# Optimization experiments

Measured on AMD Instinct MI355X. Metric: run time of the kernel, lower is better.

The kernel has to match this reference:

```python
import jax, jax.numpy as jnp
import numpy as np
import math

INPUT_SIZE = 4096
NUM_NEURONS = 4096
ATTN_SIZE = 64
BATCH = 8192


def setup_inputs() -> dict:
    key = jax.random.key(0)
    ks = jax.random.split(key, 10)
    lim_in = 1.0 / math.sqrt(INPUT_SIZE)
    lim_a = 1.0 / math.sqrt(ATTN_SIZE)
    x = jax.random.normal(ks[0], (BATCH, INPUT_SIZE), dtype=jnp.float32)
    # attention linears (torch default uniform(-1/sqrt(fan_in), ...))
    Wq = jax.random.uniform(ks[1], (ATTN_SIZE, INPUT_SIZE), jnp.float32, -lim_in, lim_in)
    bq = jnp.zeros((ATTN_SIZE,), jnp.float32)
    Wk = jax.random.uniform(ks[2], (ATTN_SIZE, INPUT_SIZE), jnp.float32, -lim_in, lim_in)
    bk = jnp.zeros((ATTN_SIZE,), jnp.float32)
    Wv = jax.random.uniform(ks[3], (ATTN_SIZE, INPUT_SIZE), jnp.float32, -lim_in, lim_in)
    bv = jnp.zeros((ATTN_SIZE,), jnp.float32)
    Wo = jax.random.uniform(ks[4], (INPUT_SIZE, ATTN_SIZE), jnp.float32, -lim_a, lim_a)
    bo = jnp.zeros((INPUT_SIZE,), jnp.float32)
    # stacked single-weight neurons: weight ~ N(0,1)*0.01, bias 0
    Wn = jax.random.normal(ks[5], (NUM_NEURONS, INPUT_SIZE), jnp.float32) * 0.01
    bn = jnp.zeros((NUM_NEURONS,), jnp.float32)
    return {"x": x, "Wq": Wq, "bq": bq, "Wk": Wk, "bk": bk,
            "Wv": Wv, "bv": bv, "Wo": Wo, "bo": bo, "Wn": Wn, "bn": bn}


def reference(x, Wq, bq, Wk, bk, Wv, bv, Wo, bo, Wn, bn):
    scale = math.sqrt(ATTN_SIZE)
    # x is treated as a length-1 "sequence" of the full feature vector: [B, 1, S]
    q = x @ Wq.T + bq            # [B, A]
    k = x @ Wk.T + bk            # [B, A]
    v = x @ Wv.T + bv            # [B, A]
    # attention over a single token: softmax of a single score == 1, kept for fidelity
    scores = jnp.sum(q * k, axis=-1, keepdims=True) / scale      # [B, 1]
    attn_w = jax.nn.softmax(scores[:, :, None], axis=-1)          # [B, 1, 1] -> all ones
    attended = attn_w[:, 0, :] * v                                # [B, A] == v
    attn_out = attended @ Wo.T + bo                               # [B, S]
    h = attn_out + x                                              # residual
    # stacked single-weight neurons == one GEMM
    out = h @ Wn.T + bn                                           # [B, N]
    return jax.nn.relu(out)
```

## Files before the change

### kernel.cpp

```cpp
#include <hip/hip_runtime.h>
#include <stdint.h>


typedef unsigned short u16;
typedef float f32x4 __attribute__((ext_vector_type(4)));
typedef __bf16 bf16x8 __attribute__((ext_vector_type(8)));
typedef u16 u16x8 __attribute__((ext_vector_type(8)));

__device__ __forceinline__ float b2f(u16 u) {
  union { unsigned int i; float f; } x; x.i = ((unsigned int)u) << 16; return x.f;
}
__device__ __forceinline__ u16 f2b(float f) {
  union { float f; unsigned int i; } x; x.f = f;
  unsigned int r = x.i + 0x7FFFu + ((x.i >> 16) & 1u);
  return (u16)(r >> 16);
}

__device__ __forceinline__ void gl_lds16(const u16* g, u16* l) {
#if __has_builtin(__builtin_amdgcn_global_load_lds)
  __builtin_amdgcn_global_load_lds((__attribute__((address_space(1))) void*)g,
                                   (__attribute__((address_space(3))) void*)l, 16, 0, 0);
#else
  int lane = threadIdx.x & 63;
  *(u16x8*)(l + lane * 8) = *(const u16x8*)g;
#endif
}

__device__ __forceinline__ f32x4 mfma16(bf16x8 a, bf16x8 b, f32x4 c) {
  return __builtin_amdgcn_mfma_f32_16x16x32_bf16(a, b, c, 0, 0, 0);
}

#define XCH 4194304L
#define WNCH 2097152L
__global__ __launch_bounds__(256) void k_cvt(
    const float* __restrict__ x, const float* __restrict__ Wn, const float* __restrict__ Wv,
    u16* __restrict__ xb, u16* __restrict__ Wnb, u16* __restrict__ Wvb) {
  long i = (long)blockIdx.x * 256 + threadIdx.x;
  const float* src; u16* dst; long off;
  if (i < XCH) { src = x; dst = xb; off = i * 8; }
  else if (i < XCH + WNCH) { src = Wn; dst = Wnb; off = (i - XCH) * 8; }
  else { src = Wv; dst = Wvb; off = (i - XCH - WNCH) * 8; }
  f32x4 a = *(const f32x4*)&src[off];
  f32x4 b = *(const f32x4*)&src[off + 4];
  u16x8 o;
#pragma unroll
  for (int e = 0; e < 4; ++e) { o[e] = f2b(a[e]); o[4 + e] = f2b(b[e]); }
  *(u16x8*)&dst[off] = o;
}

__global__ __launch_bounds__(256) void kT(const float* __restrict__ Wo, u16* __restrict__ WoT) {
  __shared__ __align__(16) u16 t[64 * 72];
  const int b = blockIdx.x;
  const int tid = threadIdx.x;
  {
    int k = tid >> 2, a0 = (tid & 3) * 16;
    const float* src = &Wo[(size_t)(b * 64 + k) * 64 + a0];
#pragma unroll
    for (int q = 0; q < 4; ++q) {
      f32x4 v = *(const f32x4*)&src[q * 4];
#pragma unroll
      for (int e = 0; e < 4; ++e) t[k * 72 + a0 + q * 4 + e] = f2b(v[e]);
    }
  }
  __syncthreads();
  {
    int a = tid >> 2, k0 = (tid & 3) * 16;
    u16x8 o0, o1;
#pragma unroll
    for (int j = 0; j < 8; ++j) o0[j] = t[(k0 + j) * 72 + a];
#pragma unroll
    for (int j = 0; j < 8; ++j) o1[j] = t[(k0 + 8 + j) * 72 + a];
    *(u16x8*)&WoT[(size_t)a * 4096 + b * 64 + k0] = o0;
    *(u16x8*)&WoT[(size_t)a * 4096 + b * 64 + k0 + 8] = o1;
  }
}

#define PBK 128
__device__ void gemm_n64(const u16* __restrict__ A, const u16* __restrict__ B,
                         u16* __restrict__ C, const float* __restrict__ bias,
                         long m0, u16* lA, u16* lB) {
  const int tid = threadIdx.x;
  const int w = tid >> 6, l = tid & 63;
  f32x4 acc[4];
#pragma unroll
  for (int nt = 0; nt < 4; ++nt) acc[nt] = (f32x4)(0.f);

  for (int k0 = 0; k0 < 4096; k0 += PBK) {
    __syncthreads();
#pragma unroll
    for (int i = 0; i < 4; ++i) {
      int row = w * 16 + i * 4 + (l >> 4);
      int p = (l & 15) ^ (i * 4 + (l >> 4));
      gl_lds16(A + (m0 + row) * (long)4096 + k0 + p * 8, lA + (w * 16 + i * 4) * PBK);
      gl_lds16(B + (long)row * 4096 + k0 + p * 8, lB + (w * 16 + i * 4) * PBK);
    }
    __syncthreads();
#pragma unroll
    for (int kk = 0; kk < 4; ++kk) {
      int slotA = ((kk * 4 + (l >> 4)) ^ (l & 15)) * 8;
      bf16x8 af = *(const bf16x8*)&lA[(w * 16 + (l & 15)) * PBK + slotA];
#pragma unroll
      for (int nt = 0; nt < 4; ++nt) {
        bf16x8 bf = *(const bf16x8*)&lB[(nt * 16 + (l & 15)) * PBK + slotA];
        acc[nt] = mfma16(af, bf, acc[nt]);
      }
    }
  }
#pragma unroll
  for (int nt = 0; nt < 4; ++nt) {
    int col = nt * 16 + (l & 15);
    float bb = bias ? bias[col] : 0.f;
#pragma unroll
    for (int r = 0; r < 4; ++r) {
      long row = m0 + w * 16 + (l >> 4) * 4 + r;
      C[row * 64 + col] = f2b(acc[nt][r] + bb);
    }
  }
}

__global__ __launch_bounds__(256, 2) void k_prep(
    const u16* __restrict__ xb, const u16* __restrict__ Wvb, const float* __restrict__ bv,
    const u16* __restrict__ Wnb, const u16* __restrict__ WoT,
    const float* __restrict__ bo, const float* __restrict__ bn,
    u16* __restrict__ V, u16* __restrict__ Wm, float* __restrict__ biasTot) {
  __shared__ __align__(16) u16 lA[64 * PBK];
  __shared__ __align__(16) u16 lB[64 * PBK];
  const int bid = blockIdx.x;
  if (bid < 128) {
    gemm_n64(xb, Wvb, V, bv, (long)bid * 64, lA, lB);
  } else if (bid < 192) {
    gemm_n64(Wnb, WoT, Wm, nullptr, (long)(bid - 128) * 64, lA, lB);
  } else {
    const int w = threadIdx.x >> 6, l = threadIdx.x & 63;
    const int n = (bid - 192) * 4 + w;
    float s = 0.f;
#pragma unroll
    for (int j = 0; j < 8; ++j) {
      int off = (j * 64 + l) * 8;
      u16x8 a = *(const u16x8*)&Wnb[(size_t)n * 4096 + off];
      f32x4 c0 = *(const f32x4*)&bo[off];
      f32x4 c1 = *(const f32x4*)&bo[off + 4];
#pragma unroll
      for (int e = 0; e < 4; ++e) s += b2f(a[e]) * c0[e] + b2f(a[4 + e]) * c1[e];
    }
#pragma unroll
    for (int o = 32; o > 0; o >>= 1) s += __shfl_xor(s, o, 64);
    if (l == 0) biasTot[n] = s + bn[n];
  }
}

__global__ __launch_bounds__(256, 2) void k_main(
    const u16* __restrict__ X, const u16* __restrict__ Wn,
    const u16* __restrict__ V, const u16* __restrict__ Wm,
    const float* __restrict__ biasTot, float* __restrict__ Out) {
  __shared__ __align__(16) u16 smem[2 * 128 * 64];
  u16* lA = smem;
  u16* lB = smem + 128 * 64;
  const int tid = threadIdx.x;
  const int w = tid >> 6, l = tid & 63;
  const int wRow = (w & 1) * 64, wCol = (w >> 1) * 64;
  const long mBase = (long)(blockIdx.x >> 5) * 128;
  const int nBase = (int)(blockIdx.x & 31) * 128;

  f32x4 acc[4][4];
#pragma unroll
  for (int mt = 0; mt < 4; ++mt)
#pragma unroll
    for (int nt = 0; nt < 4; ++nt) acc[mt][nt] = (f32x4)(0.f);

  const int srow = l >> 3;
  const int sp = ((l & 7) ^ srow) * 8;

  for (int kb = 0; kb < 65; ++kb) {
    const u16 *pA, *pB; long lda;
    if (kb < 64) { pA = X + (long)kb * 64; pB = Wn + (long)kb * 64; lda = 4096; }
    else         { pA = V;                 pB = Wm;                 lda = 64;  }
    __syncthreads();
#pragma unroll
    for (int i = 0; i < 4; ++i) {
      int row = w * 32 + i * 8 + srow;
      gl_lds16(pA + (mBase + row) * lda + sp, lA + (w * 32 + i * 8) * 64);
      gl_lds16(pB + (long)(nBase + row) * lda + sp, lB + (w * 32 + i * 8) * 64);
    }
    __syncthreads();
#pragma unroll
    for (int kk = 0; kk < 2; ++kk) {
      int slot = ((kk * 4 + (l >> 4)) ^ (l & 7)) * 8;
      bf16x8 af[4], bfr[4];
#pragma unroll
      for (int mt = 0; mt < 4; ++mt)
        af[mt] = *(const bf16x8*)&lA[(wRow + mt * 16 + (l & 15)) * 64 + slot];
#pragma unroll
      for (int nt = 0; nt < 4; ++nt)
        bfr[nt] = *(const bf16x8*)&lB[(wCol + nt * 16 + (l & 15)) * 64 + slot];
#pragma unroll
      for (int mt = 0; mt < 4; ++mt)
#pragma unroll
        for (int nt = 0; nt < 4; ++nt) acc[mt][nt] = mfma16(af[mt], bfr[nt], acc[mt][nt]);
    }
  }

  __syncthreads();
  float* eb = ((float*)smem) + w * 1024;
#pragma unroll
  for (int mt = 0; mt < 4; ++mt) {
#pragma unroll
    for (int nt = 0; nt < 4; ++nt) {
      float bt = biasTot[nBase + wCol + nt * 16 + (l & 15)];
#pragma unroll
      for (int r = 0; r < 4; ++r) {
        float val = acc[mt][nt][r] + bt;
        eb[((l >> 4) * 4 + r) * 64 + nt * 16 + (l & 15)] = fmaxf(val, 0.f);
      }
    }
    int rr = l >> 2, c0 = (l & 3) * 16;
    long grow = mBase + wRow + mt * 16 + rr;
    int gcol = nBase + wCol + c0;
    f32x4 o0 = *(const f32x4*)&eb[rr * 64 + c0];
    f32x4 o1 = *(const f32x4*)&eb[rr * 64 + c0 + 4];
    f32x4 o2 = *(const f32x4*)&eb[rr * 64 + c0 + 8];
    f32x4 o3 = *(const f32x4*)&eb[rr * 64 + c0 + 12];
    *(f32x4*)&Out[grow * 4096 + gcol] = o0;
    *(f32x4*)&Out[grow * 4096 + gcol + 4] = o1;
    *(f32x4*)&Out[grow * 4096 + gcol + 8] = o2;
    *(f32x4*)&Out[grow * 4096 + gcol + 12] = o3;
  }
}

extern "C" void kernel_launch(void* const* d_in, const int* in_sizes, int n_in,
                              void* d_out, int out_size, void* d_ws, size_t ws_size,
                              hipStream_t stream) {
  const float* x  = (const float*)d_in[0];
  const float* Wv = (const float*)d_in[5];
  const float* bv = (const float*)d_in[6];
  const float* Wo = (const float*)d_in[7];
  const float* bo = (const float*)d_in[8];
  const float* Wn = (const float*)d_in[9];
  const float* bn = (const float*)d_in[10];
  float* out = (float*)d_out;

  char* ws = (char*)d_ws;
  u16* xb  = (u16*)ws;
  u16* Wnb = (u16*)(ws + (64L << 20));
  u16* Wvb = (u16*)(ws + (96L << 20));
  u16* WoT = (u16*)(ws + (96L << 20) + (512 << 10));
  u16* V   = (u16*)(ws + (97L << 20));
  u16* Wm  = (u16*)(ws + (98L << 20));
  float* biasTot = (float*)(ws + (98L << 20) + (512 << 10));

  k_cvt<<<dim3(24704), dim3(256), 0, stream>>>(x, Wn, Wv, xb, Wnb, Wvb);
  kT<<<dim3(64), dim3(256), 0, stream>>>(Wo, WoT);
  k_prep<<<dim3(1216), dim3(256), 0, stream>>>(xb, Wvb, bv, Wnb, WoT, bo, bn, V, Wm, biasTot);
  k_main<<<dim3(2048), dim3(256), 0, stream>>>(xb, Wnb, V, Wm, biasTot, out);
}
```

Baseline: 586.8 us.

## Restructure main GEMM to 256x256 tiles with a 4-stage LDS prefetch pipeline

The main bf16 GEMM moves from 128x128 tiles with 256 threads and a single-buffer load-sync-compute loop to 256x256 tiles with 512 threads. Each wave now holds a 128x64 accumulator. Global-to-LDS loads run two stages ahead through a 4-slot ring buffer, are split between the A and B halves, and are interleaved with MFMA phases raised via setprio. The goal is to hide global memory latency and reduce operand traffic per FLOP. The cost is 128KB of LDS per block, which limits occupancy to one block per CU, and a smaller grid of 512 blocks.

```diff
diff --git a/kernel.cpp b/kernel.cpp
--- a/kernel.cpp
+++ b/kernel.cpp
@@ -149,68 +149,126 @@
   }
 }
 
-__global__ __launch_bounds__(256, 2) void k_main(
+__global__ __launch_bounds__(512, 2) void k_main(
     const u16* __restrict__ X, const u16* __restrict__ Wn,
     const u16* __restrict__ V, const u16* __restrict__ Wm,
     const float* __restrict__ biasTot, float* __restrict__ Out) {
-  __shared__ __align__(16) u16 smem[2 * 128 * 64];
-  u16* lA = smem;
-  u16* lB = smem + 128 * 64;
+  __shared__ __align__(16) u16 smem[4 * 16384];
   const int tid = threadIdx.x;
   const int w = tid >> 6, l = tid & 63;
-  const int wRow = (w & 1) * 64, wCol = (w >> 1) * 64;
-  const long mBase = (long)(blockIdx.x >> 5) * 128;
-  const int nBase = (int)(blockIdx.x & 31) * 128;
-
-  f32x4 acc[4][4];
-#pragma unroll
-  for (int mt = 0; mt < 4; ++mt)
+  const int wm = w >> 2, wn = w & 3;
+  const long mBase = (long)(blockIdx.x >> 4) * 256;
+  const int  nBase = (int)(blockIdx.x & 15) * 256;
+
+  const int rs  = l >> 2;
+  const int gsl = ((l & 3) ^ ((l >> 3) & 3)) * 8;
+  const long rA = mBase + w * 16 + rs;
+  const long rB = nBase + w * 16 + rs;
+  const u16* xA0 = X  + rA * 4096 + gsl;
+  const u16* xA1 = xA0 + 128L * 4096;
+  const u16* nB0 = Wn + rB * 4096 + gsl;
+  const u16* nB1 = nB0 + 128L * 4096;
+  const u16* vA0 = V  + rA * 64 + gsl;
+  const u16* vA1 = vA0 + 128 * 64;
+  const u16* wB0 = Wm + rB * 64 + gsl;
+  const u16* wB1 = wB0 + 128 * 64;
+  const int dA0 = w * 512;
+  const int dA1 = 4096 + dA0;
+  const int dB0 = 8192 + dA0, dB1 = 8192 + dA1;
+
+  const int frow = l & 15;
+  const int sxor = ((l >> 4) ^ ((l >> 1) & 3)) * 8;
+  const int aoffA = (wm * 128 + frow) * 32 + sxor;
+  const int aoffB = 8192 + (wn * 64 + frow) * 32 + sxor;
+
+  f32x4 acc[8][4];
+#pragma unroll
+  for (int mt = 0; mt < 8; ++mt)
 #pragma unroll
     for (int nt = 0; nt < 4; ++nt) acc[mt][nt] = (f32x4)(0.f);
 
-  const int srow = l >> 3;
-  const int sp = ((l & 7) ^ srow) * 8;
-
-  for (int kb = 0; kb < 65; ++kb) {
-    const u16 *pA, *pB; long lda;
-    if (kb < 64) { pA = X + (long)kb * 64; pB = Wn + (long)kb * 64; lda = 4096; }
-    else         { pA = V;                 pB = Wm;                 lda = 64;  }
-    __syncthreads();
-#pragma unroll
-    for (int i = 0; i < 4; ++i) {
-      int row = w * 32 + i * 8 + srow;
-      gl_lds16(pA + (mBase + row) * lda + sp, lA + (w * 32 + i * 8) * 64);
-      gl_lds16(pB + (long)(nBase + row) * lda + sp, lB + (w * 32 + i * 8) * 64);
-    }
-    __syncthreads();
-#pragma unroll
-    for (int kk = 0; kk < 2; ++kk) {
-      int slot = ((kk * 4 + (l >> 4)) ^ (l & 7)) * 8;
-      bf16x8 af[4], bfr[4];
-#pragma unroll
-      for (int mt = 0; mt < 4; ++mt)
-        af[mt] = *(const bf16x8*)&lA[(wRow + mt * 16 + (l & 15)) * 64 + slot];
-#pragma unroll
-      for (int nt = 0; nt < 4; ++nt)
-        bfr[nt] = *(const bf16x8*)&lB[(wCol + nt * 16 + (l & 15)) * 64 + slot];
-#pragma unroll
-      for (int mt = 0; mt < 4; ++mt)
-#pragma unroll
-        for (int nt = 0; nt < 4; ++nt) acc[mt][nt] = mfma16(af[mt], bfr[nt], acc[mt][nt]);
-    }
+  gl_lds16(xA0,      smem + dA0);
+  gl_lds16(xA1,      smem + dA1);
+  gl_lds16(nB0,      smem + dB0);
+  gl_lds16(nB1,      smem + dB1);
+  gl_lds16(xA0 + 32, smem + 16384 + dA0);
+  gl_lds16(xA1 + 32, smem + 16384 + dA1);
+  gl_lds16(nB0 + 32, smem + 16384 + dB0);
+  gl_lds16(nB1 + 32, smem + 16384 + dB1);
+  asm volatile("s_waitcnt vmcnt(4)" ::: "memory");
+  __builtin_amdgcn_s_barrier();
+
+  bf16x8 af[4], bq[4];
+  for (int s = 0; s < 130; ++s) {
+    const int qb = (s & 3) * 16384;
+    const int t = s + 2;
+    const int qs = (t & 3) * 16384;
+    const long ko = (long)t * 32;
+#pragma unroll
+    for (int i = 0; i < 4; ++i) af[i] = *(const bf16x8*)&smem[qb + aoffA + i * 512];
+#pragma unroll
+    for (int i = 0; i < 4; ++i) bq[i] = *(const bf16x8*)&smem[qb + aoffB + i * 512];
+    if (t < 128) {
+      gl_lds16(xA0 + ko, smem + qs + dA0);
+      gl_lds16(xA1 + ko, smem + qs + dA1);
+    } else if (t < 130) {
+      const long kv = (long)(t - 128) * 32;
+      gl_lds16(vA0 + kv, smem + qs + dA0);
+      gl_lds16(vA1 + kv, smem + qs + dA1);
+    }
+    __builtin_amdgcn_s_barrier();
+    asm volatile("s_waitcnt lgkmcnt(0)" ::: "memory");
+    __builtin_amdgcn_sched_barrier(0);
+    __builtin_amdgcn_s_setprio(1);
+#pragma unroll
+    for (int mt = 0; mt < 4; ++mt)
+#pragma unroll
+      for (int nt = 0; nt < 4; ++nt) acc[mt][nt] = mfma16(af[mt], bq[nt], acc[mt][nt]);
+    __builtin_amdgcn_s_setprio(0);
+    __builtin_amdgcn_sched_barrier(0);
+    __builtin_amdgcn_s_barrier();
+#pragma unroll
+    for (int i = 0; i < 4; ++i) af[i] = *(const bf16x8*)&smem[qb + aoffA + (4 + i) * 512];
+    if (t < 128) {
+      gl_lds16(nB0 + ko, smem + qs + dB0);
+      gl_lds16(nB1 + ko, smem + qs + dB1);
+    } else if (t < 130) {
+      const long kv = (long)(t - 128) * 32;
+      gl_lds16(wB0 + kv, smem + qs + dB0);
+      gl_lds16(wB1 + kv, smem + qs + dB1);
+    }
+    __builtin_amdgcn_s_barrier();
+    asm volatile("s_waitcnt lgkmcnt(0)" ::: "memory");
+    __builtin_amdgcn_sched_barrier(0);
+    __builtin_amdgcn_s_setprio(1);
+#pragma unroll
+    for (int mt = 0; mt < 4; ++mt)
+#pragma unroll
+      for (int nt = 0; nt < 4; ++nt) acc[4 + mt][nt] = mfma16(af[mt], bq[nt], acc[4 + mt][nt]);
+    __builtin_amdgcn_s_setprio(0);
+    __builtin_amdgcn_sched_barrier(0);
+    if (s < 128) {
+      asm volatile("s_waitcnt vmcnt(4)" ::: "memory");
+    } else if (s == 128) {
+      asm volatile("s_waitcnt vmcnt(0)" ::: "memory");
+    }
+    __builtin_amdgcn_s_barrier();
   }
 
   __syncthreads();
   float* eb = ((float*)smem) + w * 1024;
-#pragma unroll
-  for (int mt = 0; mt < 4; ++mt) {
+  const int wRow = wm * 128, wCol = wn * 64;
+  float bt[4];
+#pragma unroll
+  for (int nt = 0; nt < 4; ++nt) bt[nt] = biasTot[nBase + wCol + nt * 16 + frow];
+#pragma unroll
+  for (int mt = 0; mt < 8; ++mt) {
 #pragma unroll
     for (int nt = 0; nt < 4; ++nt) {
-      float bt = biasTot[nBase + wCol + nt * 16 + (l & 15)];
 #pragma unroll
       for (int r = 0; r < 4; ++r) {
-        float val = acc[mt][nt][r] + bt;
-        eb[((l >> 4) * 4 + r) * 64 + nt * 16 + (l & 15)] = fmaxf(val, 0.f);
+        float val = acc[mt][nt][r] + bt[nt];
+        eb[((l >> 4) * 4 + r) * 64 + nt * 16 + frow] = fmaxf(val, 0.f);
       }
     }
     int rr = l >> 2, c0 = (l & 3) * 16;
@@ -251,5 +309,5 @@
   k_cvt<<<dim3(24704), dim3(256), 0, stream>>>(x, Wn, Wv, xb, Wnb, Wvb);
   kT<<<dim3(64), dim3(256), 0, stream>>>(Wo, WoT);
   k_prep<<<dim3(1216), dim3(256), 0, stream>>>(xb, Wvb, bv, Wnb, WoT, bo, bn, V, Wm, biasTot);
-  k_main<<<dim3(2048), dim3(256), 0, stream>>>(xb, Wnb, V, Wm, biasTot, out);
-}
+  k_main<<<dim3(512), dim3(512), 0, stream>>>(xb, Wnb, V, Wm, biasTot, out);
+}
```

Measured after the change: 614.4 us. 1.05x slower.

## Fuse conversion, transpose and prep GEMMs into one pre-kernel reading fp32 directly

Applied to the files above, without the earlier changes.

Merges the fp32-to-bf16 conversion, the Wo transpose and the prep GEMMs (V = xWv^T, Wm = Wn·Wo) into a single launch. The small GEMMs now load fp32 operands and convert them in registers, with strided reads for transposed Wo, so Wv is never converted and WoT is never materialised. The aim is to cut kernel launches and serialization between them. The trade-off is that the prep GEMMs lose the async global-to-LDS loads and the Wo path uses uncoalesced strided loads. Prep and conversion blocks now also compete inside one grid.

```diff
diff --git a/kernel.cpp b/kernel.cpp
--- a/kernel.cpp
+++ b/kernel.cpp
@@ -30,57 +30,16 @@
   return __builtin_amdgcn_mfma_f32_16x16x32_bf16(a, b, c, 0, 0, 0);
 }
 
-#define XCH 4194304L
-#define WNCH 2097152L
-__global__ __launch_bounds__(256) void k_cvt(
-    const float* __restrict__ x, const float* __restrict__ Wn, const float* __restrict__ Wv,
-    u16* __restrict__ xb, u16* __restrict__ Wnb, u16* __restrict__ Wvb) {
-  long i = (long)blockIdx.x * 256 + threadIdx.x;
-  const float* src; u16* dst; long off;
-  if (i < XCH) { src = x; dst = xb; off = i * 8; }
-  else if (i < XCH + WNCH) { src = Wn; dst = Wnb; off = (i - XCH) * 8; }
-  else { src = Wv; dst = Wvb; off = (i - XCH - WNCH) * 8; }
-  f32x4 a = *(const f32x4*)&src[off];
-  f32x4 b = *(const f32x4*)&src[off + 4];
-  u16x8 o;
-#pragma unroll
-  for (int e = 0; e < 4; ++e) { o[e] = f2b(a[e]); o[4 + e] = f2b(b[e]); }
-  *(u16x8*)&dst[off] = o;
-}
-
-__global__ __launch_bounds__(256) void kT(const float* __restrict__ Wo, u16* __restrict__ WoT) {
-  __shared__ __align__(16) u16 t[64 * 72];
-  const int b = blockIdx.x;
-  const int tid = threadIdx.x;
-  {
-    int k = tid >> 2, a0 = (tid & 3) * 16;
-    const float* src = &Wo[(size_t)(b * 64 + k) * 64 + a0];
-#pragma unroll
-    for (int q = 0; q < 4; ++q) {
-      f32x4 v = *(const f32x4*)&src[q * 4];
-#pragma unroll
-      for (int e = 0; e < 4; ++e) t[k * 72 + a0 + q * 4 + e] = f2b(v[e]);
-    }
-  }
-  __syncthreads();
-  {
-    int a = tid >> 2, k0 = (tid & 3) * 16;
-    u16x8 o0, o1;
-#pragma unroll
-    for (int j = 0; j < 8; ++j) o0[j] = t[(k0 + j) * 72 + a];
-#pragma unroll
-    for (int j = 0; j < 8; ++j) o1[j] = t[(k0 + 8 + j) * 72 + a];
-    *(u16x8*)&WoT[(size_t)a * 4096 + b * 64 + k0] = o0;
-    *(u16x8*)&WoT[(size_t)a * 4096 + b * 64 + k0 + 8] = o1;
-  }
-}
-
 #define PBK 128
-__device__ void gemm_n64(const u16* __restrict__ A, const u16* __restrict__ B,
-                         u16* __restrict__ C, const float* __restrict__ bias,
-                         long m0, u16* lA, u16* lB) {
+
+template <bool BT>
+__device__ void gemm_n64_f32(const float* __restrict__ A, const float* __restrict__ B,
+                             u16* __restrict__ C, const float* __restrict__ bias,
+                             long m0, u16* lA, u16* lB) {
   const int tid = threadIdx.x;
   const int w = tid >> 6, l = tid & 63;
+  const int rg = l >> 4;
+  const int sl = l & 15;
   f32x4 acc[4];
 #pragma unroll
   for (int nt = 0; nt < 4; ++nt) acc[nt] = (f32x4)(0.f);
@@ -89,10 +48,28 @@
     __syncthreads();
 #pragma unroll
     for (int i = 0; i < 4; ++i) {
-      int row = w * 16 + i * 4 + (l >> 4);
-      int p = (l & 15) ^ (i * 4 + (l >> 4));
-      gl_lds16(A + (m0 + row) * (long)4096 + k0 + p * 8, lA + (w * 16 + i * 4) * PBK);
-      gl_lds16(B + (long)row * 4096 + k0 + p * 8, lB + (w * 16 + i * 4) * PBK);
+      int row = w * 16 + i * 4 + rg;
+      int p = sl ^ (i * 4 + rg);
+      const float* ga = &A[(m0 + row) * 4096L + k0 + p * 8];
+      f32x4 a0 = *(const f32x4*)ga;
+      f32x4 a1 = *(const f32x4*)(ga + 4);
+      u16x8 av;
+#pragma unroll
+      for (int e = 0; e < 4; ++e) { av[e] = f2b(a0[e]); av[4 + e] = f2b(a1[e]); }
+      *(u16x8*)&lA[(w * 16 + i * 4) * PBK + l * 8] = av;
+      u16x8 bv;
+      if (!BT) {
+        const float* gb = &B[(long)row * 4096 + k0 + p * 8];
+        f32x4 b0 = *(const f32x4*)gb;
+        f32x4 b1 = *(const f32x4*)(gb + 4);
+#pragma unroll
+        for (int e = 0; e < 4; ++e) { bv[e] = f2b(b0[e]); bv[4 + e] = f2b(b1[e]); }
+      } else {
+        const float* gb = &B[(long)(k0 + p * 8) * 64 + row];
+#pragma unroll
+        for (int e = 0; e < 8; ++e) bv[e] = f2b(gb[e * 64]);
+      }
+      *(u16x8*)&lB[(w * 16 + i * 4) * PBK + l * 8] = bv;
     }
     __syncthreads();
 #pragma unroll
@@ -118,34 +95,50 @@
   }
 }
 
-__global__ __launch_bounds__(256, 2) void k_prep(
-    const u16* __restrict__ xb, const u16* __restrict__ Wvb, const float* __restrict__ bv,
-    const u16* __restrict__ Wnb, const u16* __restrict__ WoT,
-    const float* __restrict__ bo, const float* __restrict__ bn,
+#define XCH 4194304L
+#define WNCH 2097152L
+#define AUXB 1216
+__global__ __launch_bounds__(256) void k_pre(
+    const float* __restrict__ x, const float* __restrict__ Wn,
+    const float* __restrict__ Wv, const float* __restrict__ Wo,
+    const float* __restrict__ bv, const float* __restrict__ bo, const float* __restrict__ bn,
+    u16* __restrict__ xb, u16* __restrict__ Wnb,
     u16* __restrict__ V, u16* __restrict__ Wm, float* __restrict__ biasTot) {
   __shared__ __align__(16) u16 lA[64 * PBK];
   __shared__ __align__(16) u16 lB[64 * PBK];
   const int bid = blockIdx.x;
   if (bid < 128) {
-    gemm_n64(xb, Wvb, V, bv, (long)bid * 64, lA, lB);
+    gemm_n64_f32<false>(x, Wv, V, bv, (long)bid * 64, lA, lB);
   } else if (bid < 192) {
-    gemm_n64(Wnb, WoT, Wm, nullptr, (long)(bid - 128) * 64, lA, lB);
-  } else {
+    gemm_n64_f32<true>(Wn, Wo, Wm, nullptr, (long)(bid - 128) * 64, lA, lB);
+  } else if (bid < AUXB) {
     const int w = threadIdx.x >> 6, l = threadIdx.x & 63;
     const int n = (bid - 192) * 4 + w;
     float s = 0.f;
 #pragma unroll
     for (int j = 0; j < 8; ++j) {
       int off = (j * 64 + l) * 8;
-      u16x8 a = *(const u16x8*)&Wnb[(size_t)n * 4096 + off];
+      f32x4 a0 = *(const f32x4*)&Wn[(size_t)n * 4096 + off];
+      f32x4 a1 = *(const f32x4*)&Wn[(size_t)n * 4096 + off + 4];
       f32x4 c0 = *(const f32x4*)&bo[off];
       f32x4 c1 = *(const f32x4*)&bo[off + 4];
 #pragma unroll
-      for (int e = 0; e < 4; ++e) s += b2f(a[e]) * c0[e] + b2f(a[4 + e]) * c1[e];
+      for (int e = 0; e < 4; ++e) s += a0[e] * c0[e] + a1[e] * c1[e];
     }
 #pragma unroll
     for (int o = 32; o > 0; o >>= 1) s += __shfl_xor(s, o, 64);
     if (l == 0) biasTot[n] = s + bn[n];
+  } else {
+    long i = (long)(bid - AUXB) * 256 + threadIdx.x;
+    const float* src; u16* dst; long off;
+    if (i < XCH) { src = x; dst = xb; off = i * 8; }
+    else { src = Wn; dst = Wnb; off = (i - XCH) * 8; }
+    f32x4 a = *(const f32x4*)&src[off];
+    f32x4 b = *(const f32x4*)&src[off + 4];
+    u16x8 o;
+#pragma unroll
+    for (int e = 0; e < 4; ++e) { o[e] = f2b(a[e]); o[4 + e] = f2b(b[e]); }
+    *(u16x8*)&dst[off] = o;
   }
 }
 
@@ -242,14 +235,11 @@
   char* ws = (char*)d_ws;
   u16* xb  = (u16*)ws;
   u16* Wnb = (u16*)(ws + (64L << 20));
-  u16* Wvb = (u16*)(ws + (96L << 20));
-  u16* WoT = (u16*)(ws + (96L << 20) + (512 << 10));
-  u16* V   = (u16*)(ws + (97L << 20));
-  u16* Wm  = (u16*)(ws + (98L << 20));
-  float* biasTot = (float*)(ws + (98L << 20) + (512 << 10));
-
-  k_cvt<<<dim3(24704), dim3(256), 0, stream>>>(x, Wn, Wv, xb, Wnb, Wvb);
-  kT<<<dim3(64), dim3(256), 0, stream>>>(Wo, WoT);
-  k_prep<<<dim3(1216), dim3(256), 0, stream>>>(xb, Wvb, bv, Wnb, WoT, bo, bn, V, Wm, biasTot);
+  u16* V   = (u16*)(ws + (96L << 20));
+  u16* Wm  = (u16*)(ws + (97L << 20));
+  float* biasTot = (float*)(ws + (97L << 20) + (512 << 10));
+
+  k_pre<<<dim3(AUXB + 24576), dim3(256), 0, stream>>>(
+      x, Wn, Wv, Wo, bv, bo, bn, xb, Wnb, V, Wm, biasTot);
   k_main<<<dim3(2048), dim3(256), 0, stream>>>(xb, Wnb, V, Wm, biasTot, out);
 }
```

After: 698.6 us. +19.0%, slower.
